# Performance work log

Measured on AMD Instinct MI355X. Metric: run time of the kernel, lower is better.

## Reference

```python
import jax, jax.numpy as jnp
import numpy as np
from jax import lax

B, L, D, F, K = 16, 1024, 384, 1536, 3
MAX_DUR = 10          # clamp on per-token duration (makes output length static)
T_OUT = L * MAX_DUR   # padded expanded length
ALPHA = 1.0
EPS = 1e-5


def conv1d_same(x_ncl, w, b):
    # x_ncl: [B, Cin, L], w: [Cout, Cin, K]
    y = lax.conv_general_dilated(x_ncl, w, window_strides=(1,), padding='SAME',
                                 dimension_numbers=('NCH', 'OIH', 'NCH'))
    return y + b[None, :, None]


def conv_block(x, wA, bA, wB, bB):
    # x: [B, L, D] -> Conv(D->F) ReLU Conv(F->D) ReLU -> [B, L, D]
    h = x.transpose(0, 2, 1)
    h = jax.nn.relu(conv1d_same(h, wA, bA))
    h = jax.nn.relu(conv1d_same(h, wB, bB))
    return h.transpose(0, 2, 1)


def layernorm(x, g, b):
    mu = jnp.mean(x, axis=-1, keepdims=True)
    var = jnp.var(x, axis=-1, keepdims=True)
    return (x - mu) * lax.rsqrt(var + EPS) * g + b


def setup_inputs() -> dict:
    key = jax.random.key(0)
    ks = jax.random.split(key, 8)
    s = 0.02
    return {
        'y': jax.random.normal(ks[0], (B, L, D), jnp.float32),
        'token_lengths': jax.random.randint(ks[1], (B,), 1, L + 1).astype(jnp.int32),
        'w1a': jax.random.normal(ks[2], (F, D, K), jnp.float32) * s,
        'b1a': jnp.zeros((F,), jnp.float32),
        'w1b': jax.random.normal(ks[3], (D, F, K), jnp.float32) * s,
        'b1b': jnp.zeros((D,), jnp.float32),
        'g1': jnp.ones((D,), jnp.float32),
        'be1': jnp.zeros((D,), jnp.float32),
        'w2a': jax.random.normal(ks[4], (F, D, K), jnp.float32) * s,
        'b2a': jnp.zeros((F,), jnp.float32),
        'w2b': jax.random.normal(ks[5], (D, F, K), jnp.float32) * s,
        'b2b': jnp.zeros((D,), jnp.float32),
        'g2': jnp.ones((D,), jnp.float32),
        'be2': jnp.zeros((D,), jnp.float32),
        'wl': jax.random.normal(ks[6], (D, 1), jnp.float32) * s,
        'bl': jnp.zeros((1,), jnp.float32),
    }


def reference(y, token_lengths, w1a, b1a, w1b, b1b, g1, be1,
              w2a, b2a, w2b, b2b, g2, be2, wl, bl):
    # DurationPredictor (eval mode: dropout is identity)
    h = conv_block(y, w1a, b1a, w1b, b1b)
    h = layernorm(h, g1, be1)
    h = conv_block(h, w2a, b2a, w2b, b2b)
    h = layernorm(h, g2, be2)
    preds = h @ wl + bl                      # [B, L, 1]

    # lengths = round(alpha * exp(preds)), masked to valid tokens, clamped
    lns = jnp.round(ALPHA * jnp.exp(preds[..., 0]))
    lns = jnp.clip(lns, 0, MAX_DUR).astype(jnp.int32)        # [B, L]
    mask = jnp.arange(L)[None, :] < token_lengths[:, None]
    lns = jnp.where(mask, lns, 0)

    # ragged repeat_interleave + pad, fully vectorized:
    # output frame t maps to token idx = searchsorted(cumsum(lns), t, 'right')
    csum = jnp.cumsum(lns, axis=1)                            # [B, L]
    totals = csum[:, -1]                                      # [B]
    t = jnp.arange(T_OUT, dtype=jnp.int32)
    idx = jax.vmap(lambda c: jnp.searchsorted(c, t, side='right'))(csum)  # [B, T_OUT]
    idx = jnp.minimum(idx, L - 1)
    gathered = jnp.take_along_axis(y, idx[..., None], axis=1)  # [B, T_OUT, D]
    valid = t[None, :] < totals[:, None]
    enlarged = jnp.where(valid[..., None], gathered, 0.0)
    return enlarged, totals
```

## Files before the change

### kernel.cpp

```cpp
#include <hip/hip_runtime.h>
#include <hip/hip_bf16.h>

#define BB 16
#define LL 1024
#define DD 384
#define FF 1536
#define KK 3
#define T_OUT 10240
#define MAX_DUR 10

#define PADL 1026
#define LO_SCALE 2048.0f
#define LO_INV   4.8828125e-4f

typedef _Float16 f16x8 __attribute__((ext_vector_type(8)));
typedef float    f32x4 __attribute__((ext_vector_type(4)));

__device__ __forceinline__ void gll16(const void* g, void* l) {
    __builtin_amdgcn_global_load_lds(
        (const __attribute__((address_space(1))) void*)g,
        (__attribute__((address_space(3))) void*)l, 16, 0, 0);
}

__device__ __forceinline__ void split_write(float v, _Float16* hi, _Float16* lo, size_t off) {
    _Float16 h = (_Float16)v;
    hi[off] = h;
    lo[off] = (_Float16)((v - (float)h) * LO_SCALE);
}

__device__ __forceinline__ float split_read(const _Float16* hi, const _Float16* lo, size_t off) {
    return (float)hi[off] + (float)lo[off] * LO_INV;
}

__global__ void prep_w(const float* __restrict__ w1a, const float* __restrict__ w1b,
                       const float* __restrict__ w2a, const float* __restrict__ w2b,
                       _Float16* __restrict__ base) {
    const int total = FF * 3 * DD;
    int id = blockIdx.x * 256 + threadIdx.x;
    int which = id / total;
    int rid = id - which * total;
    if (which >= 4) return;
    const float* w; _Float16 *hi, *lo; int O, I;
    const size_t WN = (size_t)FF * DD * KK;
    if (which == 0)      { w = w1a; O = FF; I = DD; hi = base;          lo = base + WN; }
    else if (which == 1) { w = w1b; O = DD; I = FF; hi = base + 2 * WN; lo = base + 3 * WN; }
    else if (which == 2) { w = w2a; O = FF; I = DD; hi = base + 4 * WN; lo = base + 5 * WN; }
    else                 { w = w2b; O = DD; I = FF; hi = base + 6 * WN; lo = base + 7 * WN; }
    int e = rid & 7;
    int lane = (rid >> 3) & 63;
    int rest = rid >> 9;
    int nKT = (3 * I) >> 5;
    int ktl = rest % nKT;
    int ot = rest / nKT;
    int o = ot * 16 + (lane & 15);
    int koff = ((lane >> 4) << 3) + e;
    int kseg = ktl % 3;
    int i = (ktl / 3) * 32 + koff;
    float v = w[(o * I + i) * 3 + kseg];
    split_write(v, hi, lo, rid);
}

__global__ void prep_y(const float* __restrict__ y, _Float16* __restrict__ shi,
                       _Float16* __restrict__ slo, _Float16* __restrict__ h1hi,
                       _Float16* __restrict__ h1lo) {
    const int SNc = BB * PADL * DD;
    int id = blockIdx.x * 256 + threadIdx.x;
    if (id < SNc) {
        int d = id % DD;
        int r = id / DD;
        int b = r / PADL;
        int lr = r - b * PADL;
        float v = 0.f;
        if (lr >= 1 && lr <= LL) v = y[((size_t)(b << 10) + (lr - 1)) * DD + d];
        split_write(v, shi, slo, id);
        return;
    }
    int id2 = id - SNc;
    if (id2 >= BB * 2 * FF) return;
    int b = id2 / (2 * FF);
    int rem = id2 - b * 2 * FF;
    int row = (rem / FF) ? (PADL - 1) : 0;
    int c = rem % FF;
    size_t off = (size_t)(b * PADL + row) * FF + c;
    h1hi[off] = (_Float16)0.f;
    h1lo[off] = (_Float16)0.f;
}

__global__ __launch_bounds__(256, 2) void gemm_split(
        const _Float16* __restrict__ Ahi, const _Float16* __restrict__ Alo,
        const _Float16* __restrict__ WfH, const _Float16* __restrict__ WfL,
        const float* __restrict__ bias,
        _Float16* __restrict__ O0hi, _Float16* __restrict__ O0lo,
        _Float16* __restrict__ O1hi, _Float16* __restrict__ O1lo,
        int Cin, int Cout, int nKTper, int nN, int blocksPerHalf, int doRelu) {
    __shared__ _Float16 lds_h[32768];
    const int tid = threadIdx.x;
    const int lane = tid & 63;
    const int w = tid >> 6;
    const int lm = lane & 15, lq = lane >> 4;
    const int nKTfull = (3 * Cin) >> 5;
    const int half = blockIdx.x / blocksPerHalf;
    const int t2in = blockIdx.x - half * blocksPerHalf;
    const int xcd = t2in & 7;
    const int t2 = t2in >> 3;
    const int g  = t2 / (4 * nN);
    const int r  = t2 - g * (4 * nN);
    const int n_t = r >> 2;
    const int mi  = r & 3;
    const int m_t = ((g * 4 + mi) << 3) + xcd;
    const int m0 = m_t << 7;
    const int n0 = n_t << 7;
    const int b = m0 >> 10;
    const int l0 = m0 & 1023;
    const int rowBase = b * PADL + l0;
    const int wm = (w >> 1) * 64, wn = (w & 1) * 64;
    const int ktBegin = half * nKTper;
    const int ktEnd = ktBegin + nKTper;

    f32x4 accM[4][4], accC[4][4];
    const f32x4 zz = {0.f, 0.f, 0.f, 0.f};
    #pragma unroll
    for (int i = 0; i < 4; ++i)
        #pragma unroll
        for (int jj = 0; jj < 4; ++jj) { accM[i][jj] = zz; accC[i][jj] = zz; }

    auto stageA = [&](int kt, int ph, int sub) {
        int kseg = kt % 3;
        int d0 = (kt / 3) << 5;
        #pragma unroll
        for (int it = 0; it < 2; ++it) {
            int s = (w * 2 + it) * 64 + lane;
            int p = s >> 3, sl = s & 7;
            int t = sl ^ (p & 7);
            int m = p * 2 + (t >> 2);
            int k8 = t & 3;
            size_t aoff = (size_t)(rowBase + m + kseg) * Cin + d0 + k8 * 8;
            _Float16* lbase = lds_h + ph * 16384 + sub * 8192 + (w * 2 + it) * 512;
            gll16(Ahi + aoff, lbase);
            gll16(Alo + aoff, lbase + 4096);
        }
    };
    auto loadB = [&](int kt, f16x8* bH, f16x8* bL) {
        #pragma unroll
        for (int jj = 0; jj < 4; ++jj) {
            int ntg = (n0 + wn + jj * 16) >> 4;
            size_t boff = (((size_t)ntg * nKTfull + kt) * 64 + lane) * 8;
            bH[jj] = *(const f16x8*)(WfH + boff);
            bL[jj] = *(const f16x8*)(WfL + boff);
        }
    };
    auto compute = [&](int ph, int sub, const f16x8* bH, const f16x8* bL) {
        const _Float16* lb = lds_h + ph * 16384 + sub * 8192;
        #pragma unroll
        for (int i = 0; i < 4; ++i) {
            int m = wm + i * 16 + lm;
            int p = m >> 1;
            int sl = (((m & 1) << 2) | lq) ^ (p & 7);
            int off = p * 64 + sl * 8;
            f16x8 aH = *(const f16x8*)(lb + off);
            f16x8 aL = *(const f16x8*)(lb + 4096 + off);
            #pragma unroll
            for (int jj = 0; jj < 4; ++jj) {
                accM[i][jj] = __builtin_amdgcn_mfma_f32_16x16x32_f16(aH, bH[jj], accM[i][jj], 0, 0, 0);
                accC[i][jj] = __builtin_amdgcn_mfma_f32_16x16x32_f16(aH, bL[jj], accC[i][jj], 0, 0, 0);
                accC[i][jj] = __builtin_amdgcn_mfma_f32_16x16x32_f16(aL, bH[jj], accC[i][jj], 0, 0, 0);
            }
        }
    };

    f16x8 bH[4], bL[4];
    stageA(ktBegin, 0, 0);
    stageA(ktBegin + 1, 0, 1);
    loadB(ktBegin, bH, bL);
    int ph = 0;
    for (int kt = ktBegin; kt < ktEnd; kt += 2) {
        __syncthreads();
        if (kt + 2 < ktEnd) { stageA(kt + 2, ph ^ 1, 0); stageA(kt + 3, ph ^ 1, 1); }
        compute(ph, 0, bH, bL);
        loadB(kt + 1, bH, bL);
        compute(ph, 1, bH, bL);
        if (kt + 2 < ktEnd) loadB(kt + 2, bH, bL);
        ph ^= 1;
    }
    _Float16* oh = half ? O1hi : O0hi;
    _Float16* ol = half ? O1lo : O0lo;
    #pragma unroll
    for (int i = 0; i < 4; ++i)
        #pragma unroll
        for (int jj = 0; jj < 4; ++jj) {
            int n_g = n0 + wn + jj * 16 + lm;
            float bv = doRelu ? bias[n_g] : 0.f;
            #pragma unroll
            for (int rr = 0; rr < 4; ++rr) {
                int l = l0 + wm + i * 16 + lq * 4 + rr;
                float v = accM[i][jj][rr] + accC[i][jj][rr] * LO_INV + bv;
                if (doRelu) v = fmaxf(v, 0.f);
                size_t off = (size_t)(b * PADL + 1 + l) * Cout + n_g;
                split_write(v, oh, ol, off);
            }
        }
}

__global__ __launch_bounds__(128) void reduce_ln_k(
        _Float16* __restrict__ P0hi, _Float16* __restrict__ P0lo,
        const _Float16* __restrict__ P1hi, const _Float16* __restrict__ P1lo,
        const float* __restrict__ bias, const float* __restrict__ g,
        const float* __restrict__ be) {
    const int row = blockIdx.x;
    const int b = row >> 10, l = row & 1023;
    const size_t base = (size_t)(b * PADL + 1 + l) * DD;
    const int tid = threadIdx.x;
    float v0 = split_read(P0hi, P0lo, base + tid)       + split_read(P1hi, P1lo, base + tid)       + bias[tid];
    float v1 = split_read(P0hi, P0lo, base + tid + 128) + split_read(P1hi, P1lo, base + tid + 128) + bias[tid + 128];
    float v2 = split_read(P0hi, P0lo, base + tid + 256) + split_read(P1hi, P1lo, base + tid + 256) + bias[tid + 256];
    v0 = fmaxf(v0, 0.f); v1 = fmaxf(v1, 0.f); v2 = fmaxf(v2, 0.f);

    __shared__ float sh[2];
    float s = v0 + v1 + v2;
    #pragma unroll
    for (int o = 32; o > 0; o >>= 1) s += __shfl_down(s, o, 64);
    if ((tid & 63) == 0) sh[tid >> 6] = s;
    __syncthreads();
    float mu = (sh[0] + sh[1]) * (1.f / DD);
    __syncthreads();
    float d0 = v0 - mu, d1 = v1 - mu, d2 = v2 - mu;
    float q = d0 * d0 + d1 * d1 + d2 * d2;
    #pragma unroll
    for (int o = 32; o > 0; o >>= 1) q += __shfl_down(q, o, 64);
    if ((tid & 63) == 0) sh[tid >> 6] = q;
    __syncthreads();
    float var = (sh[0] + sh[1]) * (1.f / DD);
    float rs = rsqrtf(var + 1e-5f);
    split_write(d0 * rs * g[tid] + be[tid], P0hi, P0lo, base + tid);
    split_write(d1 * rs * g[tid + 128] + be[tid + 128], P0hi, P0lo, base + tid + 128);
    split_write(d2 * rs * g[tid + 256] + be[tid + 256], P0hi, P0lo, base + tid + 256);
}

__global__ __launch_bounds__(128) void reduce_ln_pred_k(
        const _Float16* __restrict__ P0hi, const _Float16* __restrict__ P0lo,
        const _Float16* __restrict__ P1hi, const _Float16* __restrict__ P1lo,
        const float* __restrict__ bias, const float* __restrict__ g,
        const float* __restrict__ be, const float* __restrict__ wl,
        const float* __restrict__ bl, const int* __restrict__ token_lengths,
        int* __restrict__ lns) {
    const int row = blockIdx.x;
    const int b = row >> 10, l = row & 1023;
    const size_t base = (size_t)(b * PADL + 1 + l) * DD;
    const int tid = threadIdx.x;
    float v0 = split_read(P0hi, P0lo, base + tid)       + split_read(P1hi, P1lo, base + tid)       + bias[tid];
    float v1 = split_read(P0hi, P0lo, base + tid + 128) + split_read(P1hi, P1lo, base + tid + 128) + bias[tid + 128];
    float v2 = split_read(P0hi, P0lo, base + tid + 256) + split_read(P1hi, P1lo, base + tid + 256) + bias[tid + 256];
    v0 = fmaxf(v0, 0.f); v1 = fmaxf(v1, 0.f); v2 = fmaxf(v2, 0.f);

    __shared__ float sh[2];
    float s = v0 + v1 + v2;
    #pragma unroll
    for (int o = 32; o > 0; o >>= 1) s += __shfl_down(s, o, 64);
    if ((tid & 63) == 0) sh[tid >> 6] = s;
    __syncthreads();
    float mu = (sh[0] + sh[1]) * (1.f / DD);
    __syncthreads();
    float d0 = v0 - mu, d1 = v1 - mu, d2 = v2 - mu;
    float q = d0 * d0 + d1 * d1 + d2 * d2;
    #pragma unroll
    for (int o = 32; o > 0; o >>= 1) q += __shfl_down(q, o, 64);
    if ((tid & 63) == 0) sh[tid >> 6] = q;
    __syncthreads();
    float var = (sh[0] + sh[1]) * (1.f / DD);
    float rs = rsqrtf(var + 1e-5f);
    __syncthreads();
    float p = (d0 * rs * g[tid]       + be[tid])       * wl[tid]
            + (d1 * rs * g[tid + 128] + be[tid + 128]) * wl[tid + 128]
            + (d2 * rs * g[tid + 256] + be[tid + 256]) * wl[tid + 256];
    #pragma unroll
    for (int o = 32; o > 0; o >>= 1) p += __shfl_down(p, o, 64);
    if ((tid & 63) == 0) sh[tid >> 6] = p;
    __syncthreads();
    if (tid == 0) {
        float pred = sh[0] + sh[1] + bl[0];
        float e = expf(pred);
        float r = rintf(e);
        r = fminf(fmaxf(r, 0.f), (float)MAX_DUR);
        int v = (int)r;
        if (l >= token_lengths[b]) v = 0;
        lns[row] = v;
    }
}

__global__ __launch_bounds__(1024) void cumsum_k(
        const int* __restrict__ lns, int* __restrict__ csum,
        float* __restrict__ totals_out) {
    __shared__ int s[1024];
    const int b = blockIdx.x, tid = threadIdx.x;
    s[tid] = lns[(b << 10) + tid];
    __syncthreads();
    #pragma unroll
    for (int o = 1; o < 1024; o <<= 1) {
        int t = (tid >= o) ? s[tid - o] : 0;
        __syncthreads();
        s[tid] += t;
        __syncthreads();
    }
    csum[(b << 10) + tid] = s[tid];
    if (tid == 1023) totals_out[b] = (float)s[1023];
}

__global__ __launch_bounds__(256) void idx_k(
        const int* __restrict__ csum, int* __restrict__ idxArr) {
    int id = blockIdx.x * 256 + threadIdx.x;
    if (id >= BB * T_OUT) return;
    int b = id / T_OUT, t = id - b * T_OUT;
    const int* c = csum + (b << 10);
    int total = c[1023];
    int r = -1;
    if (t < total) {
        int lo = 0, hi = 1024;
        while (lo < hi) {
            int mid = (lo + hi) >> 1;
            if (c[mid] <= t) lo = mid + 1; else hi = mid;
        }
        r = min(lo, LL - 1);
    }
    idxArr[id] = r;
}

__global__ __launch_bounds__(256) void gather_k(
        const float* __restrict__ y, const int* __restrict__ idxArr,
        float* __restrict__ out) {
    int gid = blockIdx.x * 256 + threadIdx.x;
    int c4 = gid % 96;
    int rest = gid / 96;
    int t = rest % T_OUT;
    int b = rest / T_OUT;
    int r = idxArr[b * T_OUT + t];
    float4 v = make_float4(0.f, 0.f, 0.f, 0.f);
    if (r >= 0) v = *(const float4*)(y + ((size_t)((b << 10) + r)) * DD + (c4 << 2));
    *(float4*)(out + ((size_t)b * T_OUT + t) * DD + (c4 << 2)) = v;
}

extern "C" void kernel_launch(void* const* d_in, const int* in_sizes, int n_in,
                              void* d_out, int out_size, void* d_ws, size_t ws_size,
                              hipStream_t stream) {
    const float* y   = (const float*)d_in[0];
    const int*   tok = (const int*)d_in[1];
    const float* w1a = (const float*)d_in[2];
    const float* b1a = (const float*)d_in[3];
    const float* w1b = (const float*)d_in[4];
    const float* b1b = (const float*)d_in[5];
    const float* g1  = (const float*)d_in[6];
    const float* be1 = (const float*)d_in[7];
    const float* w2a = (const float*)d_in[8];
    const float* b2a = (const float*)d_in[9];
    const float* w2b = (const float*)d_in[10];
    const float* b2b = (const float*)d_in[11];
    const float* g2  = (const float*)d_in[12];
    const float* be2 = (const float*)d_in[13];
    const float* wl  = (const float*)d_in[14];
    const float* bl  = (const float*)d_in[15];

    float* out = (float*)d_out;

    const size_t WN   = (size_t)FF * DD * KK;
    const size_t SN   = (size_t)BB * PADL * DD;
    const size_t H1N  = (size_t)BB * PADL * FF;
    _Float16* wsh = (_Float16*)d_ws;
    _Float16* Wh1a = wsh;            _Float16* Wl1a = Wh1a + WN;
    _Float16* Wh1b = Wl1a + WN;      _Float16* Wl1b = Wh1b + WN;
    _Float16* Wh2a = Wl1b + WN;      _Float16* Wl2a = Wh2a + WN;
    _Float16* Wh2b = Wl2a + WN;      _Float16* Wl2b = Wh2b + WN;
    _Float16* Shi  = Wl2b + WN;      _Float16* Slo  = Shi + SN;
    _Float16* H1hi = Slo + SN;       _Float16* H1lo = H1hi + H1N;
    _Float16* P1hi = H1lo + H1N;     _Float16* P1lo = P1hi + SN;
    int* lns    = (int*)(P1lo + SN);
    int* csum   = lns + BB * LL;
    int* idxArr = csum + BB * LL;

    const int M = BB * LL;

    prep_w<<<(4 * FF * 3 * DD) / 256, 256, 0, stream>>>(w1a, w1b, w2a, w2b, wsh);
    prep_y<<<(int)((SN + BB * 2 * FF + 255) / 256), 256, 0, stream>>>(y, Shi, Slo, H1hi, H1lo);

    gemm_split<<<(M / 128) * (FF / 128), 256, 0, stream>>>(
        Shi, Slo, Wh1a, Wl1a, b1a, H1hi, H1lo, H1hi, H1lo,
        DD, FF, (3 * DD) >> 5, FF / 128, (M / 128) * (FF / 128), 1);
    gemm_split<<<2 * (M / 128) * (DD / 128), 256, 0, stream>>>(
        H1hi, H1lo, Wh1b, Wl1b, b1b, Shi, Slo, P1hi, P1lo,
        FF, DD, ((3 * FF) >> 5) / 2, DD / 128, (M / 128) * (DD / 128), 0);
    reduce_ln_k<<<M, 128, 0, stream>>>(Shi, Slo, P1hi, P1lo, b1b, g1, be1);

    gemm_split<<<(M / 128) * (FF / 128), 256, 0, stream>>>(
        Shi, Slo, Wh2a, Wl2a, b2a, H1hi, H1lo, H1hi, H1lo,
        DD, FF, (3 * DD) >> 5, FF / 128, (M / 128) * (FF / 128), 1);
    gemm_split<<<2 * (M / 128) * (DD / 128), 256, 0, stream>>>(
        H1hi, H1lo, Wh2b, Wl2b, b2b, Shi, Slo, P1hi, P1lo,
        FF, DD, ((3 * FF) >> 5) / 2, DD / 128, (M / 128) * (DD / 128), 0);
    reduce_ln_pred_k<<<M, 128, 0, stream>>>(Shi, Slo, P1hi, P1lo, b2b, g2, be2, wl, bl, tok, lns);

    cumsum_k<<<BB, 1024, 0, stream>>>(lns, csum, out + (size_t)BB * T_OUT * DD);
    idx_k<<<(BB * T_OUT + 255) / 256, 256, 0, stream>>>(csum, idxArr);
    {
        long long n = (long long)BB * T_OUT * 96;
        gather_k<<<(int)((n + 255) / 256), 256, 0, stream>>>(y, idxArr, out);
    }
}
```

Measured before the change: 1.049 ms.

## Split F->D conv GEMM K into four parts, single-stage LDS pipeline, partials in output buffer

The F->D convolution GEMMs now split the reduction dimension four ways instead of two, so four times as many blocks run on the narrow output. The four partial sums are written into the not-yet-used output buffer and summed in the layernorm kernels. The GEMM main loop now moves one K-tile per iteration with a 2-buffer LDS layout of half the previous size, which may raise occupancy. It also hoists the A fragments before the MFMA loop. The trade-off is more partial-sum traffic and less prefetch depth per iteration.

```diff
diff --git a/kernel.cpp b/kernel.cpp
--- a/kernel.cpp
+++ b/kernel.cpp
@@ -40,12 +40,12 @@
     int which = id / total;
     int rid = id - which * total;
     if (which >= 4) return;
-    const float* w; _Float16 *hi, *lo; int O, I;
+    const float* w; _Float16 *hi, *lo; int I;
     const size_t WN = (size_t)FF * DD * KK;
-    if (which == 0)      { w = w1a; O = FF; I = DD; hi = base;          lo = base + WN; }
-    else if (which == 1) { w = w1b; O = DD; I = FF; hi = base + 2 * WN; lo = base + 3 * WN; }
-    else if (which == 2) { w = w2a; O = FF; I = DD; hi = base + 4 * WN; lo = base + 5 * WN; }
-    else                 { w = w2b; O = DD; I = FF; hi = base + 6 * WN; lo = base + 7 * WN; }
+    if (which == 0)      { w = w1a; I = DD; hi = base;          lo = base + WN; }
+    else if (which == 1) { w = w1b; I = FF; hi = base + 2 * WN; lo = base + 3 * WN; }
+    else if (which == 2) { w = w2a; I = DD; hi = base + 4 * WN; lo = base + 5 * WN; }
+    else                 { w = w2b; I = FF; hi = base + 6 * WN; lo = base + 7 * WN; }
     int e = rid & 7;
     int lane = (rid >> 3) & 63;
     int rest = rid >> 9;
@@ -90,10 +90,10 @@
         const _Float16* __restrict__ Ahi, const _Float16* __restrict__ Alo,
         const _Float16* __restrict__ WfH, const _Float16* __restrict__ WfL,
         const float* __restrict__ bias,
-        _Float16* __restrict__ O0hi, _Float16* __restrict__ O0lo,
-        _Float16* __restrict__ O1hi, _Float16* __restrict__ O1lo,
+        _Float16* __restrict__ Ohi, _Float16* __restrict__ Olo,
+        size_t halfStride,
         int Cin, int Cout, int nKTper, int nN, int blocksPerHalf, int doRelu) {
-    __shared__ _Float16 lds_h[32768];
+    __shared__ _Float16 lds_h[16384];
     const int tid = threadIdx.x;
     const int lane = tid & 63;
     const int w = tid >> 6;
@@ -124,7 +124,7 @@
         #pragma unroll
         for (int jj = 0; jj < 4; ++jj) { accM[i][jj] = zz; accC[i][jj] = zz; }
 
-    auto stageA = [&](int kt, int ph, int sub) {
+    auto stageA = [&](int kt, int nxt) {
         int kseg = kt % 3;
         int d0 = (kt / 3) << 5;
         #pragma unroll
@@ -135,12 +135,17 @@
             int m = p * 2 + (t >> 2);
             int k8 = t & 3;
             size_t aoff = (size_t)(rowBase + m + kseg) * Cin + d0 + k8 * 8;
-            _Float16* lbase = lds_h + ph * 16384 + sub * 8192 + (w * 2 + it) * 512;
+            _Float16* lbase = lds_h + nxt * 8192 + (size_t)(w * 2 + it) * 512;
             gll16(Ahi + aoff, lbase);
             gll16(Alo + aoff, lbase + 4096);
         }
     };
-    auto loadB = [&](int kt, f16x8* bH, f16x8* bL) {
+
+    stageA(ktBegin, 0);
+    for (int kt = ktBegin; kt < ktEnd; ++kt) {
+        const int cur = (kt - ktBegin) & 1;
+        __syncthreads();
+        f16x8 bH[4], bL[4];
         #pragma unroll
         for (int jj = 0; jj < 4; ++jj) {
             int ntg = (n0 + wn + jj * 16) >> 4;
@@ -148,42 +153,29 @@
             bH[jj] = *(const f16x8*)(WfH + boff);
             bL[jj] = *(const f16x8*)(WfL + boff);
         }
-    };
-    auto compute = [&](int ph, int sub, const f16x8* bH, const f16x8* bL) {
-        const _Float16* lb = lds_h + ph * 16384 + sub * 8192;
+        if (kt + 1 < ktEnd) stageA(kt + 1, cur ^ 1);
+        const _Float16* lb = lds_h + cur * 8192;
+        f16x8 aH[4], aL[4];
         #pragma unroll
         for (int i = 0; i < 4; ++i) {
             int m = wm + i * 16 + lm;
             int p = m >> 1;
             int sl = (((m & 1) << 2) | lq) ^ (p & 7);
             int off = p * 64 + sl * 8;
-            f16x8 aH = *(const f16x8*)(lb + off);
-            f16x8 aL = *(const f16x8*)(lb + 4096 + off);
+            aH[i] = *(const f16x8*)(lb + off);
+            aL[i] = *(const f16x8*)(lb + 4096 + off);
+        }
+        #pragma unroll
+        for (int jj = 0; jj < 4; ++jj)
             #pragma unroll
-            for (int jj = 0; jj < 4; ++jj) {
-                accM[i][jj] = __builtin_amdgcn_mfma_f32_16x16x32_f16(aH, bH[jj], accM[i][jj], 0, 0, 0);
-                accC[i][jj] = __builtin_amdgcn_mfma_f32_16x16x32_f16(aH, bL[jj], accC[i][jj], 0, 0, 0);
-                accC[i][jj] = __builtin_amdgcn_mfma_f32_16x16x32_f16(aL, bH[jj], accC[i][jj], 0, 0, 0);
+            for (int i = 0; i < 4; ++i) {
+                accM[i][jj] = __builtin_amdgcn_mfma_f32_16x16x32_f16(aH[i], bH[jj], accM[i][jj], 0, 0, 0);
+                accC[i][jj] = __builtin_amdgcn_mfma_f32_16x16x32_f16(aH[i], bL[jj], accC[i][jj], 0, 0, 0);
+                accC[i][jj] = __builtin_amdgcn_mfma_f32_16x16x32_f16(aL[i], bH[jj], accC[i][jj], 0, 0, 0);
             }
-        }
-    };
-
-    f16x8 bH[4], bL[4];
-    stageA(ktBegin, 0, 0);
-    stageA(ktBegin + 1, 0, 1);
-    loadB(ktBegin, bH, bL);
-    int ph = 0;
-    for (int kt = ktBegin; kt < ktEnd; kt += 2) {
-        __syncthreads();
-        if (kt + 2 < ktEnd) { stageA(kt + 2, ph ^ 1, 0); stageA(kt + 3, ph ^ 1, 1); }
-        compute(ph, 0, bH, bL);
-        loadB(kt + 1, bH, bL);
-        compute(ph, 1, bH, bL);
-        if (kt + 2 < ktEnd) loadB(kt + 2, bH, bL);
-        ph ^= 1;
-    }
-    _Float16* oh = half ? O1hi : O0hi;
-    _Float16* ol = half ? O1lo : O0lo;
+    }
+    _Float16* oh = Ohi + (size_t)half * halfStride;
+    _Float16* ol = Olo + (size_t)half * halfStride;
     #pragma unroll
     for (int i = 0; i < 4; ++i)
         #pragma unroll
@@ -202,17 +194,24 @@
 }
 
 __global__ __launch_bounds__(128) void reduce_ln_k(
-        _Float16* __restrict__ P0hi, _Float16* __restrict__ P0lo,
-        const _Float16* __restrict__ P1hi, const _Float16* __restrict__ P1lo,
+        const _Float16* __restrict__ Pbase, size_t halfStride,
+        _Float16* __restrict__ Shi, _Float16* __restrict__ Slo,
         const float* __restrict__ bias, const float* __restrict__ g,
         const float* __restrict__ be) {
     const int row = blockIdx.x;
     const int b = row >> 10, l = row & 1023;
+    const size_t SNc = (size_t)BB * PADL * DD;
     const size_t base = (size_t)(b * PADL + 1 + l) * DD;
     const int tid = threadIdx.x;
-    float v0 = split_read(P0hi, P0lo, base + tid)       + split_read(P1hi, P1lo, base + tid)       + bias[tid];
-    float v1 = split_read(P0hi, P0lo, base + tid + 128) + split_read(P1hi, P1lo, base + tid + 128) + bias[tid + 128];
-    float v2 = split_read(P0hi, P0lo, base + tid + 256) + split_read(P1hi, P1lo, base + tid + 256) + bias[tid + 256];
+    float v0 = bias[tid], v1 = bias[tid + 128], v2 = bias[tid + 256];
+    #pragma unroll
+    for (int h = 0; h < 4; ++h) {
+        const _Float16* ph = Pbase + (size_t)h * halfStride;
+        const _Float16* pl = ph + SNc;
+        v0 += split_read(ph, pl, base + tid);
+        v1 += split_read(ph, pl, base + tid + 128);
+        v2 += split_read(ph, pl, base + tid + 256);
+    }
     v0 = fmaxf(v0, 0.f); v1 = fmaxf(v1, 0.f); v2 = fmaxf(v2, 0.f);
 
     __shared__ float sh[2];
@@ -231,25 +230,31 @@
     __syncthreads();
     float var = (sh[0] + sh[1]) * (1.f / DD);
     float rs = rsqrtf(var + 1e-5f);
-    split_write(d0 * rs * g[tid] + be[tid], P0hi, P0lo, base + tid);
-    split_write(d1 * rs * g[tid + 128] + be[tid + 128], P0hi, P0lo, base + tid + 128);
-    split_write(d2 * rs * g[tid + 256] + be[tid + 256], P0hi, P0lo, base + tid + 256);
+    split_write(d0 * rs * g[tid] + be[tid], Shi, Slo, base + tid);
+    split_write(d1 * rs * g[tid + 128] + be[tid + 128], Shi, Slo, base + tid + 128);
+    split_write(d2 * rs * g[tid + 256] + be[tid + 256], Shi, Slo, base + tid + 256);
 }
 
 __global__ __launch_bounds__(128) void reduce_ln_pred_k(
-        const _Float16* __restrict__ P0hi, const _Float16* __restrict__ P0lo,
-        const _Float16* __restrict__ P1hi, const _Float16* __restrict__ P1lo,
+        const _Float16* __restrict__ Pbase, size_t halfStride,
         const float* __restrict__ bias, const float* __restrict__ g,
         const float* __restrict__ be, const float* __restrict__ wl,
         const float* __restrict__ bl, const int* __restrict__ token_lengths,
         int* __restrict__ lns) {
     const int row = blockIdx.x;
     const int b = row >> 10, l = row & 1023;
+    const size_t SNc = (size_t)BB * PADL * DD;
     const size_t base = (size_t)(b * PADL + 1 + l) * DD;
     const int tid = threadIdx.x;
-    float v0 = split_read(P0hi, P0lo, base + tid)       + split_read(P1hi, P1lo, base + tid)       + bias[tid];
-    float v1 = split_read(P0hi, P0lo, base + tid + 128) + split_read(P1hi, P1lo, base + tid + 128) + bias[tid + 128];
-    float v2 = split_read(P0hi, P0lo, base + tid + 256) + split_read(P1hi, P1lo, base + tid + 256) + bias[tid + 256];
+    float v0 = bias[tid], v1 = bias[tid + 128], v2 = bias[tid + 256];
+    #pragma unroll
+    for (int h = 0; h < 4; ++h) {
+        const _Float16* ph = Pbase + (size_t)h * halfStride;
+        const _Float16* pl = ph + SNc;
+        v0 += split_read(ph, pl, base + tid);
+        v1 += split_read(ph, pl, base + tid + 128);
+        v2 += split_read(ph, pl, base + tid + 256);
+    }
     v0 = fmaxf(v0, 0.f); v1 = fmaxf(v1, 0.f); v2 = fmaxf(v2, 0.f);
 
     __shared__ float sh[2];
@@ -370,31 +375,36 @@
     _Float16* Wh2b = Wl2a + WN;      _Float16* Wl2b = Wh2b + WN;
     _Float16* Shi  = Wl2b + WN;      _Float16* Slo  = Shi + SN;
     _Float16* H1hi = Slo + SN;       _Float16* H1lo = H1hi + H1N;
-    _Float16* P1hi = H1lo + H1N;     _Float16* P1lo = P1hi + SN;
-    int* lns    = (int*)(P1lo + SN);
+    int* lns    = (int*)(H1lo + H1N);
     int* csum   = lns + BB * LL;
     int* idxArr = csum + BB * LL;
 
+    _Float16* Pbase = (_Float16*)d_out;
+    const size_t halfStride = 2 * SN;
+
     const int M = BB * LL;
 
     prep_w<<<(4 * FF * 3 * DD) / 256, 256, 0, stream>>>(w1a, w1b, w2a, w2b, wsh);
     prep_y<<<(int)((SN + BB * 2 * FF + 255) / 256), 256, 0, stream>>>(y, Shi, Slo, H1hi, H1lo);
 
-    gemm_split<<<(M / 128) * (FF / 128), 256, 0, stream>>>(
-        Shi, Slo, Wh1a, Wl1a, b1a, H1hi, H1lo, H1hi, H1lo,
-        DD, FF, (3 * DD) >> 5, FF / 128, (M / 128) * (FF / 128), 1);
-    gemm_split<<<2 * (M / 128) * (DD / 128), 256, 0, stream>>>(
-        H1hi, H1lo, Wh1b, Wl1b, b1b, Shi, Slo, P1hi, P1lo,
-        FF, DD, ((3 * FF) >> 5) / 2, DD / 128, (M / 128) * (DD / 128), 0);
-    reduce_ln_k<<<M, 128, 0, stream>>>(Shi, Slo, P1hi, P1lo, b1b, g1, be1);
-
-    gemm_split<<<(M / 128) * (FF / 128), 256, 0, stream>>>(
-        Shi, Slo, Wh2a, Wl2a, b2a, H1hi, H1lo, H1hi, H1lo,
-        DD, FF, (3 * DD) >> 5, FF / 128, (M / 128) * (FF / 128), 1);
-    gemm_split<<<2 * (M / 128) * (DD / 128), 256, 0, stream>>>(
-        H1hi, H1lo, Wh2b, Wl2b, b2b, Shi, Slo, P1hi, P1lo,
-        FF, DD, ((3 * FF) >> 5) / 2, DD / 128, (M / 128) * (DD / 128), 0);
-    reduce_ln_pred_k<<<M, 128, 0, stream>>>(Shi, Slo, P1hi, P1lo, b2b, g2, be2, wl, bl, tok, lns);
+    const int ffBlocks = (M / 128) * (FF / 128);
+    const int ddBlocksPerHalf = (M / 128) * (DD / 128);
+
+    gemm_split<<<ffBlocks, 256, 0, stream>>>(
+        Shi, Slo, Wh1a, Wl1a, b1a, H1hi, H1lo, 0,
+        DD, FF, (3 * DD) >> 5, FF / 128, ffBlocks, 1);
+    gemm_split<<<4 * ddBlocksPerHalf, 256, 0, stream>>>(
+        H1hi, H1lo, Wh1b, Wl1b, b1b, Pbase, Pbase + SN, halfStride,
+        FF, DD, ((3 * FF) >> 5) / 4, DD / 128, ddBlocksPerHalf, 0);
+    reduce_ln_k<<<M, 128, 0, stream>>>(Pbase, halfStride, Shi, Slo, b1b, g1, be1);
+
+    gemm_split<<<ffBlocks, 256, 0, stream>>>(
+        Shi, Slo, Wh2a, Wl2a, b2a, H1hi, H1lo, 0,
+        DD, FF, (3 * DD) >> 5, FF / 128, ffBlocks, 1);
+    gemm_split<<<4 * ddBlocksPerHalf, 256, 0, stream>>>(
+        H1hi, H1lo, Wh2b, Wl2b, b2b, Pbase, Pbase + SN, halfStride,
+        FF, DD, ((3 * FF) >> 5) / 4, DD / 128, ddBlocksPerHalf, 0);
+    reduce_ln_pred_k<<<M, 128, 0, stream>>>(Pbase, halfStride, b2b, g2, be2, wl, bl, tok, lns);
 
     cumsum_k<<<BB, 1024, 0, stream>>>(lns, csum, out + (size_t)BB * T_OUT * DD);
     idx_k<<<(BB * T_OUT + 255) / 256, 256, 0, stream>>>(csum, idxArr);
```

Result: no change. 1.051 ms (+0.2%).
